# Kernel tuning notes

Measured on AMD Instinct MI355X. Metric: run time of the kernel, lower is better.

The kernel has to match this reference:

```python
import jax, jax.numpy as jnp
import numpy as np

V, OOV, E, HE, HD, N, S, TD = 50000, 50, 256, 512, 512, 32, 400, 30
PAD_INF = -1e10


def _gru_step(h, x, Wih, Whh, bih, bhh):
    gi = x @ Wih.T + bih            # [N,3H]
    gh = h @ Whh.T + bhh
    ir, iz, inn = jnp.split(gi, 3, axis=-1)
    hr, hz, hn = jnp.split(gh, 3, axis=-1)
    r = jax.nn.sigmoid(ir + hr)
    z = jax.nn.sigmoid(iz + hz)
    n = jnp.tanh(inn + r * hn)
    return (1.0 - z) * n + z * h


def setup_inputs() -> dict:
    key = jax.random.key(0)
    ks = iter(jax.random.split(key, 40))
    def rn(shape, s=0.05):
        return s * jax.random.normal(next(ks), shape, dtype=jnp.float32)
    return {
        "src_ids": jax.random.randint(next(ks), (N, S), 0, V),
        "src_mask": jnp.ones((N, S), jnp.float32),
        "trg_ids": jax.random.randint(next(ks), (N, TD), 0, V),
        "ptr_src_idx": jax.random.randint(next(ks), (N, S), 0, V + OOV),
        "embed": rn((V, E), 0.1),
        "Wih_f": rn((3 * HE, E)), "Whh_f": rn((3 * HE, HE)),
        "bih_f": rn((3 * HE,)), "bhh_f": rn((3 * HE,)),
        "Wih_b": rn((3 * HE, E)), "Whh_b": rn((3 * HE, HE)),
        "bih_b": rn((3 * HE,)), "bhh_b": rn((3 * HE,)),
        "Wih_d": rn((3 * HD, E)), "Whh_d": rn((3 * HD, HD)),
        "bih_d": rn((3 * HD,)), "bhh_d": rn((3 * HD,)),
        "Wk": rn((2 * HE, HD)), "Wd": rn((HD, HD)), "battn": rn((HD,)), "v": rn((HD,)),
        "W1": rn((2 * HE + HD, HD)), "b1": rn((HD,)),
        "W2": rn((HD, V)), "b2": rn((V,)),
        "Wp": rn((2 * HE + HD + E, 1)), "bp": rn((1,)),
    }


def reference(src_ids, src_mask, trg_ids, ptr_src_idx, embed,
              Wih_f, Whh_f, bih_f, bhh_f, Wih_b, Whh_b, bih_b, bhh_b,
              Wih_d, Whh_d, bih_d, bhh_d, Wk, Wd, battn, v,
              W1, b1, W2, b2, Wp, bp):
    n = src_ids.shape[0]
    # ---- bidirectional GRU encoder ----
    xt = jnp.swapaxes(embed[src_ids], 0, 1)        # [S,N,E]
    h0 = jnp.zeros((n, HE), jnp.float32)
    def fstep(h, xi):
        h2 = _gru_step(h, xi, Wih_f, Whh_f, bih_f, bhh_f)
        return h2, h2
    def bstep(h, xi):
        h2 = _gru_step(h, xi, Wih_b, Whh_b, bih_b, bhh_b)
        return h2, h2
    _, hf = jax.lax.scan(fstep, h0, xt)
    _, hb = jax.lax.scan(bstep, h0, xt[::-1])
    enc = jnp.swapaxes(jnp.concatenate([hf, hb[::-1]], axis=-1), 0, 1)  # [N,S,2HE]

    key_proj = enc @ Wk                             # [N,S,HD] precomputed attn keys
    mask_add = (1.0 - src_mask) * PAD_INF           # [N,S]
    rows = jnp.arange(n)[:, None]

    trg_emb = jnp.swapaxes(embed[trg_ids], 0, 1)    # [TD,N,E]
    hd0 = jnp.zeros((n, HD), jnp.float32)

    def dstep(h, xi):
        h = _gru_step(h, xi, Wih_d, Whh_d, bih_d, bhh_d)
        # additive attention
        e = jnp.tanh(key_proj + (h @ Wd + battn)[:, None, :]) @ v + mask_add  # [N,S]
        attn = jax.nn.softmax(e, axis=-1)
        ctx = jnp.einsum('ns,nsd->nd', attn, enc)                # [N,2HE]
        concat = jnp.concatenate([h, ctx], axis=-1)              # [N,2HE+HD]
        gen = jax.nn.softmax((concat @ W1 + b1) @ W2 + b2, axis=-1)  # [N,V]
        gen_ext = jnp.concatenate([gen, jnp.zeros((n, OOV), gen.dtype)], axis=-1)
        p_gen = jax.nn.sigmoid(jnp.concatenate([xi, ctx, h], axis=-1) @ Wp + bp)  # [N,1]
        out = (p_gen * gen_ext).at[rows, ptr_src_idx].add((1.0 - p_gen) * attn)
        return h, out

    _, dists = jax.lax.scan(dstep, hd0, trg_emb)    # [TD,N,V+OOV]
    return jnp.swapaxes(dists, 0, 1)                # [N,TD,V+OOV]
```

## Files before the change

kernel.cpp:

```cpp
#include <hip/hip_runtime.h>
#include <math.h>

#define VSZ 50000
#define OOVN 50
#define VE 50050
#define EMB 256
#define HE 512
#define HD 512
#define NB 32
#define SRC 400
#define TDD 30
#define G3 1536
#define ENC_PER_DIR 128
#define DEC_NBLK 128

__device__ __forceinline__ float sigmf(float x) { return 1.f / (1.f + expf(-x)); }

__global__ __launch_bounds__(256) void transpose_kernel(const float* __restrict__ in,
                                                        float* __restrict__ out,
                                                        int rows, int cols) {
    int idx = blockIdx.x * 256 + threadIdx.x;
    if (idx >= rows * cols) return;
    int r = idx / cols, c = idx % cols;
    out[c * rows + r] = in[idx];
}

__global__ __launch_bounds__(256) void gi_kernel(const int* __restrict__ ids,
                                                 const float* __restrict__ embed,
                                                 const float* __restrict__ WihT,
                                                 const float* __restrict__ bih,
                                                 float* __restrict__ gi, int steps) {
    __shared__ float sx[16][EMB];
    __shared__ int stok[16];
    int tid = threadIdx.x;
    int g0 = blockIdx.x * 16;
    if (tid < 16) {
        int row = g0 + tid;
        int s = row / NB, n = row % NB;
        stok[tid] = ids[n * steps + s];
    }
    __syncthreads();
    for (int r = 0; r < 16; ++r) sx[r][tid] = embed[(size_t)stok[r] * EMB + tid];
    __syncthreads();
    int c = blockIdx.y * 256 + tid;
    float b = bih[c];
    float acc[16];
#pragma unroll
    for (int r = 0; r < 16; ++r) acc[r] = b;
    for (int e = 0; e < EMB; e += 4) {
        float w0 = WihT[(size_t)(e + 0) * G3 + c];
        float w1 = WihT[(size_t)(e + 1) * G3 + c];
        float w2 = WihT[(size_t)(e + 2) * G3 + c];
        float w3 = WihT[(size_t)(e + 3) * G3 + c];
#pragma unroll
        for (int r = 0; r < 16; ++r) {
            float4 x4 = *(const float4*)&sx[r][e];
            acc[r] += x4.x * w0 + x4.y * w1 + x4.z * w2 + x4.w * w3;
        }
    }
#pragma unroll
    for (int r = 0; r < 16; ++r) gi[(size_t)(g0 + r) * G3 + c] = acc[r];
}

__global__ __launch_bounds__(512) void enc_scan_kernel(
    const float* __restrict__ giF, const float* __restrict__ giB,
    const float* __restrict__ WhhF, const float* __restrict__ WhhB,
    const float* __restrict__ bhhF, const float* __restrict__ bhhB,
    float* __restrict__ hF0, float* __restrict__ hF1,
    float* __restrict__ hB0, float* __restrict__ hB1,
    float* __restrict__ enc, unsigned int* __restrict__ cnt) {
    const int bid = blockIdx.x;
    const int z = bid >> 7;
    const int j0 = (bid & 127) * 4;
    const float* gi  = z ? giB : giF;
    const float* Whh = z ? WhhB : WhhF;
    const float* bhh = z ? bhhB : bhhF;
    float* hbuf[2];
    hbuf[0] = z ? hB0 : hF0;
    hbuf[1] = z ? hB1 : hF1;
    unsigned int* cntd = cnt + (size_t)z * 512;

    __shared__ float hlds[32 * 576];

    const int tid = threadIdx.x;
    const int jl = tid & 3;
    const int kh = (tid >> 2) & 15;
    const int ng = tid >> 6;
    const int j  = j0 + jl;
    const int kbase = kh * 36;

    float4 wreg[3][8];
#pragma unroll
    for (int g = 0; g < 3; ++g) {
        const float* wp = Whh + (size_t)(g * 512 + j) * 512 + kh * 32;
#pragma unroll
        for (int i = 0; i < 8; ++i) wreg[g][i] = *(const float4*)&wp[i * 4];
    }
    const float bR = bhh[j], bZ = bhh[512 + j], bN = bhh[1024 + j];

    for (int t = 0; t < SRC; ++t) {
        const float* hin = hbuf[t & 1];
        float* hout = hbuf[(t + 1) & 1];
        const unsigned long long* hin8 = (const unsigned long long*)hin;
        for (int idx = tid; idx < 32 * 256; idx += 512) {
            unsigned long long uv = __hip_atomic_load(&hin8[idx], __ATOMIC_RELAXED,
                                                      __HIP_MEMORY_SCOPE_AGENT);
            union { unsigned long long u; float f[2]; } cv; cv.u = uv;
            int nn = idx >> 8, kk = (idx & 255) << 1;
            int off = nn * 576 + (kk >> 5) * 36 + (kk & 31);
            hlds[off] = cv.f[0];
            hlds[off + 1] = cv.f[1];
        }
        __syncthreads();

        float aR[4] = {0.f, 0.f, 0.f, 0.f};
        float aZ[4] = {0.f, 0.f, 0.f, 0.f};
        float aN[4] = {0.f, 0.f, 0.f, 0.f};
        const float* h0p = &hlds[(ng * 4 + 0) * 576 + kbase];
        const float* h1p = &hlds[(ng * 4 + 1) * 576 + kbase];
        const float* h2p = &hlds[(ng * 4 + 2) * 576 + kbase];
        const float* h3p = &hlds[(ng * 4 + 3) * 576 + kbase];
#pragma unroll
        for (int i = 0; i < 8; ++i) {
            float4 wr = wreg[0][i], wz = wreg[1][i], wn = wreg[2][i];
            float4 ha = *(const float4*)&h0p[i * 4];
            float4 hb = *(const float4*)&h1p[i * 4];
            float4 hc = *(const float4*)&h2p[i * 4];
            float4 hd = *(const float4*)&h3p[i * 4];
            aR[0] += ha.x*wr.x + ha.y*wr.y + ha.z*wr.z + ha.w*wr.w;
            aZ[0] += ha.x*wz.x + ha.y*wz.y + ha.z*wz.z + ha.w*wz.w;
            aN[0] += ha.x*wn.x + ha.y*wn.y + ha.z*wn.z + ha.w*wn.w;
            aR[1] += hb.x*wr.x + hb.y*wr.y + hb.z*wr.z + hb.w*wr.w;
            aZ[1] += hb.x*wz.x + hb.y*wz.y + hb.z*wz.z + hb.w*wz.w;
            aN[1] += hb.x*wn.x + hb.y*wn.y + hb.z*wn.z + hb.w*wn.w;
            aR[2] += hc.x*wr.x + hc.y*wr.y + hc.z*wr.z + hc.w*wr.w;
            aZ[2] += hc.x*wz.x + hc.y*wz.y + hc.z*wz.z + hc.w*wz.w;
            aN[2] += hc.x*wn.x + hc.y*wn.y + hc.z*wn.z + hc.w*wn.w;
            aR[3] += hd.x*wr.x + hd.y*wr.y + hd.z*wr.z + hd.w*wr.w;
            aZ[3] += hd.x*wz.x + hd.y*wz.y + hd.z*wz.z + hd.w*wz.w;
            aN[3] += hd.x*wn.x + hd.y*wn.y + hd.z*wn.z + hd.w*wn.w;
        }
#pragma unroll
        for (int r = 0; r < 4; ++r) {
            aR[r] += __shfl_xor(aR[r], 4);  aR[r] += __shfl_xor(aR[r], 8);
            aR[r] += __shfl_xor(aR[r], 16); aR[r] += __shfl_xor(aR[r], 32);
            aZ[r] += __shfl_xor(aZ[r], 4);  aZ[r] += __shfl_xor(aZ[r], 8);
            aZ[r] += __shfl_xor(aZ[r], 16); aZ[r] += __shfl_xor(aZ[r], 32);
            aN[r] += __shfl_xor(aN[r], 4);  aN[r] += __shfl_xor(aN[r], 8);
            aN[r] += __shfl_xor(aN[r], 16); aN[r] += __shfl_xor(aN[r], 32);
        }
        if (kh == 0) {
            int s = z ? (SRC - 1 - t) : t;
#pragma unroll
            for (int r = 0; r < 4; ++r) {
                int n = ng * 4 + r;
                const float* gir = gi + (size_t)(s * NB + n) * G3;
                float rr  = sigmf(gir[j] + bR + aR[r]);
                float zz  = sigmf(gir[512 + j] + bZ + aZ[r]);
                float nn2 = tanhf(gir[1024 + j] + bN + rr * aN[r]);
                float hp  = hlds[n * 576 + (j >> 5) * 36 + (j & 31)];
                float hnew = (1.f - zz) * nn2 + zz * hp;
                __hip_atomic_store(&hout[n * 512 + j], hnew, __ATOMIC_RELAXED,
                                   __HIP_MEMORY_SCOPE_AGENT);
                enc[(size_t)(n * SRC + s) * 1024 + z * 512 + j] = hnew;
            }
        }
        __syncthreads();
        if (tid == 0) {
            __hip_atomic_fetch_add(&cntd[t], 1u, __ATOMIC_RELAXED, __HIP_MEMORY_SCOPE_AGENT);
            while (__hip_atomic_load(&cntd[t], __ATOMIC_RELAXED, __HIP_MEMORY_SCOPE_AGENT)
                   < (unsigned)ENC_PER_DIR)
                __builtin_amdgcn_s_sleep(2);
        }
        __syncthreads();
    }
}

__global__ __launch_bounds__(512) void dec_scan_kernel(
    const float* __restrict__ gi, const float* __restrict__ Whh,
    const float* __restrict__ bhh, const float* __restrict__ h0,
    float* __restrict__ hall, unsigned int* __restrict__ cnt) {
    const int j0 = blockIdx.x * 4;
    __shared__ float hlds[32 * 576];
    const int tid = threadIdx.x;
    const int jl = tid & 3;
    const int kh = (tid >> 2) & 15;
    const int ng = tid >> 6;
    const int j  = j0 + jl;
    const int kbase = kh * 36;

    float4 wreg[3][8];
#pragma unroll
    for (int g = 0; g < 3; ++g) {
        const float* wp = Whh + (size_t)(g * 512 + j) * 512 + kh * 32;
#pragma unroll
        for (int i = 0; i < 8; ++i) wreg[g][i] = *(const float4*)&wp[i * 4];
    }
    const float bR = bhh[j], bZ = bhh[512 + j], bN = bhh[1024 + j];

    for (int t = 0; t < TDD; ++t) {
        const float* hin = t ? (hall + (size_t)(t - 1) * NB * 512) : h0;
        float* hout = hall + (size_t)t * NB * 512;
        const unsigned long long* hin8 = (const unsigned long long*)hin;
        for (int idx = tid; idx < 32 * 256; idx += 512) {
            unsigned long long uv = __hip_atomic_load(&hin8[idx], __ATOMIC_RELAXED,
                                                      __HIP_MEMORY_SCOPE_AGENT);
            union { unsigned long long u; float f[2]; } cv; cv.u = uv;
            int nn = idx >> 8, kk = (idx & 255) << 1;
            int off = nn * 576 + (kk >> 5) * 36 + (kk & 31);
            hlds[off] = cv.f[0];
            hlds[off + 1] = cv.f[1];
        }
        __syncthreads();

        float aR[4] = {0.f, 0.f, 0.f, 0.f};
        float aZ[4] = {0.f, 0.f, 0.f, 0.f};
        float aN[4] = {0.f, 0.f, 0.f, 0.f};
        const float* h0p = &hlds[(ng * 4 + 0) * 576 + kbase];
        const float* h1p = &hlds[(ng * 4 + 1) * 576 + kbase];
        const float* h2p = &hlds[(ng * 4 + 2) * 576 + kbase];
        const float* h3p = &hlds[(ng * 4 + 3) * 576 + kbase];
#pragma unroll
        for (int i = 0; i < 8; ++i) {
            float4 wr = wreg[0][i], wz = wreg[1][i], wn = wreg[2][i];
            float4 ha = *(const float4*)&h0p[i * 4];
            float4 hb = *(const float4*)&h1p[i * 4];
            float4 hc = *(const float4*)&h2p[i * 4];
            float4 hd = *(const float4*)&h3p[i * 4];
            aR[0] += ha.x*wr.x + ha.y*wr.y + ha.z*wr.z + ha.w*wr.w;
            aZ[0] += ha.x*wz.x + ha.y*wz.y + ha.z*wz.z + ha.w*wz.w;
            aN[0] += ha.x*wn.x + ha.y*wn.y + ha.z*wn.z + ha.w*wn.w;
            aR[1] += hb.x*wr.x + hb.y*wr.y + hb.z*wr.z + hb.w*wr.w;
            aZ[1] += hb.x*wz.x + hb.y*wz.y + hb.z*wz.z + hb.w*wz.w;
            aN[1] += hb.x*wn.x + hb.y*wn.y + hb.z*wn.z + hb.w*wn.w;
            aR[2] += hc.x*wr.x + hc.y*wr.y + hc.z*wr.z + hc.w*wr.w;
            aZ[2] += hc.x*wz.x + hc.y*wz.y + hc.z*wz.z + hc.w*wz.w;
            aN[2] += hc.x*wn.x + hc.y*wn.y + hc.z*wn.z + hc.w*wn.w;
            aR[3] += hd.x*wr.x + hd.y*wr.y + hd.z*wr.z + hd.w*wr.w;
            aZ[3] += hd.x*wz.x + hd.y*wz.y + hd.z*wz.z + hd.w*wz.w;
            aN[3] += hd.x*wn.x + hd.y*wn.y + hd.z*wn.z + hd.w*wn.w;
        }
#pragma unroll
        for (int r = 0; r < 4; ++r) {
            aR[r] += __shfl_xor(aR[r], 4);  aR[r] += __shfl_xor(aR[r], 8);
            aR[r] += __shfl_xor(aR[r], 16); aR[r] += __shfl_xor(aR[r], 32);
            aZ[r] += __shfl_xor(aZ[r], 4);  aZ[r] += __shfl_xor(aZ[r], 8);
            aZ[r] += __shfl_xor(aZ[r], 16); aZ[r] += __shfl_xor(aZ[r], 32);
            aN[r] += __shfl_xor(aN[r], 4);  aN[r] += __shfl_xor(aN[r], 8);
            aN[r] += __shfl_xor(aN[r], 16); aN[r] += __shfl_xor(aN[r], 32);
        }
        if (kh == 0) {
#pragma unroll
            for (int r = 0; r < 4; ++r) {
                int n = ng * 4 + r;
                const float* gir = gi + (size_t)(t * NB + n) * G3;
                float rr  = sigmf(gir[j] + bR + aR[r]);
                float zz  = sigmf(gir[512 + j] + bZ + aZ[r]);
                float nn2 = tanhf(gir[1024 + j] + bN + rr * aN[r]);
                float hp  = hlds[n * 576 + (j >> 5) * 36 + (j & 31)];
                float hnew = (1.f - zz) * nn2 + zz * hp;
                __hip_atomic_store(&hout[n * 512 + j], hnew, __ATOMIC_RELAXED,
                                   __HIP_MEMORY_SCOPE_AGENT);
            }
        }
        __syncthreads();
        if (tid == 0) {
            __hip_atomic_fetch_add(&cnt[t], 1u, __ATOMIC_RELAXED, __HIP_MEMORY_SCOPE_AGENT);
            while (__hip_atomic_load(&cnt[t], __ATOMIC_RELAXED, __HIP_MEMORY_SCOPE_AGENT)
                   < (unsigned)DEC_NBLK)
                __builtin_amdgcn_s_sleep(2);
        }
        __syncthreads();
    }
}

__global__ __launch_bounds__(256) void keyproj_kernel(const float* __restrict__ enc,
                                                      const float* __restrict__ Wk,
                                                      float* __restrict__ kp) {
    __shared__ float sx[8][1024];
    int tid = threadIdx.x;
    int g0 = blockIdx.x * 8;
    for (int i = tid; i < 8 * 1024; i += 256)
        sx[i >> 10][i & 1023] = enc[(size_t)(g0 + (i >> 10)) * 1024 + (i & 1023)];
    __syncthreads();
    int c = blockIdx.y * 256 + tid;
    float acc[8];
#pragma unroll
    for (int r = 0; r < 8; ++r) acc[r] = 0.f;
    for (int k = 0; k < 1024; k += 4) {
        float w0 = Wk[(size_t)(k + 0) * 512 + c];
        float w1 = Wk[(size_t)(k + 1) * 512 + c];
        float w2 = Wk[(size_t)(k + 2) * 512 + c];
        float w3 = Wk[(size_t)(k + 3) * 512 + c];
#pragma unroll
        for (int r = 0; r < 8; ++r) {
            float4 x4 = *(const float4*)&sx[r][k];
            acc[r] += x4.x * w0 + x4.y * w1 + x4.z * w2 + x4.w * w3;
        }
    }
#pragma unroll
    for (int r = 0; r < 8; ++r) kp[(size_t)(g0 + r) * 512 + c] = acc[r];
}

__global__ __launch_bounds__(256) void qall_kernel(const float* __restrict__ hall,
                                                   const float* __restrict__ Wd,
                                                   const float* __restrict__ battn,
                                                   float* __restrict__ qall) {
    __shared__ float sx[8][512];
    int tid = threadIdx.x;
    int g0 = blockIdx.x * 8;
    for (int i = tid; i < 8 * 512; i += 256)
        sx[i >> 9][i & 511] = hall[(size_t)(g0 + (i >> 9)) * 512 + (i & 511)];
    __syncthreads();
    int c = blockIdx.y * 256 + tid;
    float b = battn[c];
    float acc[8];
#pragma unroll
    for (int r = 0; r < 8; ++r) acc[r] = b;
    for (int k = 0; k < 512; k += 4) {
        float w0 = Wd[(size_t)(k + 0) * 512 + c];
        float w1 = Wd[(size_t)(k + 1) * 512 + c];
        float w2 = Wd[(size_t)(k + 2) * 512 + c];
        float w3 = Wd[(size_t)(k + 3) * 512 + c];
#pragma unroll
        for (int r = 0; r < 8; ++r) {
            float4 x4 = *(const float4*)&sx[r][k];
            acc[r] += x4.x * w0 + x4.y * w1 + x4.z * w2 + x4.w * w3;
        }
    }
#pragma unroll
    for (int r = 0; r < 8; ++r) qall[(size_t)(g0 + r) * 512 + c] = acc[r];
}

__global__ __launch_bounds__(256) void escoreall_kernel(const float* __restrict__ kp,
                                                        const float* __restrict__ qall,
                                                        const float* __restrict__ vvec,
                                                        const float* __restrict__ mask,
                                                        float* __restrict__ e) {
    __shared__ float sq[512];
    int tid = threadIdx.x;
    int row0 = blockIdx.x * 4;
    int tn = row0 / SRC;
    int n = tn % NB;
    sq[tid] = qall[(size_t)tn * 512 + tid];
    sq[256 + tid] = qall[(size_t)tn * 512 + 256 + tid];
    __syncthreads();
    int w = tid >> 6, lane = tid & 63;
    int row = row0 + w;
    int s = row % SRC;
    const float* kpr = kp + (size_t)(n * SRC + s) * 512;
    float acc = 0.f;
#pragma unroll
    for (int i = 0; i < 8; ++i) {
        int d = lane + i * 64;
        acc += vvec[d] * tanhf(kpr[d] + sq[d]);
    }
    for (int off = 32; off; off >>= 1) acc += __shfl_down(acc, off, 64);
    if (lane == 0) e[row] = acc + (1.f - mask[n * SRC + s]) * (-1e10f);
}

__global__ __launch_bounds__(256) void softmaxS_kernel(float* __restrict__ e) {
    __shared__ float red[256];
    int n = blockIdx.x, tid = threadIdx.x;
    float* row = e + (size_t)n * SRC;
    float m = -3.4e38f;
    for (int s = tid; s < SRC; s += 256) m = fmaxf(m, row[s]);
    red[tid] = m; __syncthreads();
    for (int off = 128; off; off >>= 1) { if (tid < off) red[tid] = fmaxf(red[tid], red[tid + off]); __syncthreads(); }
    m = red[0]; __syncthreads();
    float sum = 0.f;
    for (int s = tid; s < SRC; s += 256) sum += expf(row[s] - m);
    red[tid] = sum; __syncthreads();
    for (int off = 128; off; off >>= 1) { if (tid < off) red[tid] += red[tid + off]; __syncthreads(); }
    float inv = 1.f / red[0]; __syncthreads();
    for (int s = tid; s < SRC; s += 256) row[s] = expf(row[s] - m) * inv;
}

__global__ __launch_bounds__(256) void ctxall_kernel(const float* __restrict__ attn,
                                                     const float* __restrict__ enc,
                                                     float* __restrict__ ctxall) {
    __shared__ float sa[TDD * SRC];
    int n = blockIdx.x, tid = threadIdx.x;
    for (int i = tid; i < TDD * SRC; i += 256) {
        int t = i / SRC, s = i - t * SRC;
        sa[i] = attn[(size_t)(t * NB + n) * SRC + s];
    }
    __syncthreads();
    int d = blockIdx.y * 256 + tid;
    const float* er = enc + (size_t)n * SRC * 1024 + d;
    float acc[TDD];
#pragma unroll
    for (int t = 0; t < TDD; ++t) acc[t] = 0.f;
    for (int s = 0; s < SRC; s += 4) {
        float e0 = er[(size_t)(s + 0) * 1024];
        float e1 = er[(size_t)(s + 1) * 1024];
        float e2 = er[(size_t)(s + 2) * 1024];
        float e3 = er[(size_t)(s + 3) * 1024];
#pragma unroll
        for (int t = 0; t < TDD; ++t) {
            float4 a4 = *(const float4*)&sa[t * SRC + s];
            acc[t] += a4.x * e0 + a4.y * e1 + a4.z * e2 + a4.w * e3;
        }
    }
#pragma unroll
    for (int t = 0; t < TDD; ++t) ctxall[(size_t)(t * NB + n) * 1024 + d] = acc[t];
}

__global__ __launch_bounds__(256) void pgenall_kernel(const int* __restrict__ trg_ids,
                                                      const float* __restrict__ embed,
                                                      const float* __restrict__ ctxall,
                                                      const float* __restrict__ hall,
                                                      const float* __restrict__ Wp,
                                                      const float* __restrict__ bp,
                                                      float* __restrict__ pgenall) {
    __shared__ float red[256];
    int tn = blockIdx.x, tid = threadIdx.x;
    int t = tn / NB, n = tn % NB;
    int tok = trg_ids[n * TDD + t];
    float acc = 0.f;
    for (int i = tid; i < 1792; i += 256) {
        float val;
        if (i < 256) val = embed[(size_t)tok * EMB + i];
        else if (i < 1280) val = ctxall[(size_t)tn * 1024 + (i - 256)];
        else val = hall[(size_t)tn * 512 + (i - 1280)];
        acc += val * Wp[i];
    }
    red[tid] = acc; __syncthreads();
    for (int off = 128; off; off >>= 1) { if (tid < off) red[tid] += red[tid + off]; __syncthreads(); }
    if (tid == 0) pgenall[tn] = 1.f / (1.f + expf(-(red[0] + bp[0])));
}

__global__ __launch_bounds__(256) void hid1all_kernel(const float* __restrict__ hall,
                                                      const float* __restrict__ ctxall,
                                                      const float* __restrict__ W1,
                                                      const float* __restrict__ b1,
                                                      float* __restrict__ hid1all) {
    __shared__ float sc[8][1536];
    int tid = threadIdx.x;
    int g0 = blockIdx.x * 8;
    for (int i = tid; i < 8 * 512; i += 256)
        sc[i >> 9][i & 511] = hall[(size_t)(g0 + (i >> 9)) * 512 + (i & 511)];
    for (int i = tid; i < 8 * 1024; i += 256)
        sc[i >> 10][512 + (i & 1023)] = ctxall[(size_t)(g0 + (i >> 10)) * 1024 + (i & 1023)];
    __syncthreads();
    int c = blockIdx.y * 256 + tid;
    float acc[8];
    float b = b1[c];
#pragma unroll
    for (int r = 0; r < 8; ++r) acc[r] = b;
    for (int k = 0; k < 1536; k += 4) {
        float w0 = W1[(size_t)(k + 0) * 512 + c];
        float w1 = W1[(size_t)(k + 1) * 512 + c];
        float w2 = W1[(size_t)(k + 2) * 512 + c];
        float w3 = W1[(size_t)(k + 3) * 512 + c];
#pragma unroll
        for (int r = 0; r < 8; ++r) {
            float4 x4 = *(const float4*)&sc[r][k];
            acc[r] += x4.x * w0 + x4.y * w1 + x4.z * w2 + x4.w * w3;
        }
    }
#pragma unroll
    for (int r = 0; r < 8; ++r) hid1all[(size_t)(g0 + r) * 512 + c] = acc[r];
}

__global__ __launch_bounds__(256) void logitsall_kernel(const float* __restrict__ hid1,
                                                        const float* __restrict__ W2,
                                                        const float* __restrict__ b2,
                                                        float* __restrict__ logits) {
    __shared__ float sh[32][512];
    int tid = threadIdx.x;
    int r0 = blockIdx.y * 32;
    for (int i = tid; i < 32 * 512; i += 256) sh[i >> 9][i & 511] = hid1[(size_t)r0 * 512 + i];
    __syncthreads();
    int j = blockIdx.x * 256 + tid;
    if (j >= VSZ) return;
    float acc[32];
#pragma unroll
    for (int r = 0; r < 32; ++r) acc[r] = 0.f;
    for (int k = 0; k < 512; k += 4) {
        float w0 = W2[(size_t)(k + 0) * VSZ + j];
        float w1 = W2[(size_t)(k + 1) * VSZ + j];
        float w2 = W2[(size_t)(k + 2) * VSZ + j];
        float w3 = W2[(size_t)(k + 3) * VSZ + j];
#pragma unroll
        for (int r = 0; r < 32; ++r) {
            float4 h4 = *(const float4*)&sh[r][k];
            acc[r] += h4.x * w0 + h4.y * w1 + h4.z * w2 + h4.w * w3;
        }
    }
    float bb = b2[j];
#pragma unroll
    for (int r = 0; r < 32; ++r) logits[(size_t)(r0 + r) * VSZ + j] = acc[r] + bb;
}

__global__ __launch_bounds__(1024) void outall_kernel(const float* __restrict__ logits,
                                                      const float* __restrict__ pgenall,
                                                      float* __restrict__ out) {
    __shared__ float red[1024];
    int tn = blockIdx.x, tid = threadIdx.x;
    int t = tn / NB, n = tn % NB;
    const float* lrow = logits + (size_t)tn * VSZ;
    float m = -3.4e38f;
    for (int j = tid; j < VSZ; j += 1024) m = fmaxf(m, lrow[j]);
    red[tid] = m; __syncthreads();
    for (int off = 512; off; off >>= 1) { if (tid < off) red[tid] = fmaxf(red[tid], red[tid + off]); __syncthreads(); }
    m = red[0]; __syncthreads();
    float sum = 0.f;
    for (int j = tid; j < VSZ; j += 1024) sum += expf(lrow[j] - m);
    red[tid] = sum; __syncthreads();
    for (int off = 512; off; off >>= 1) { if (tid < off) red[tid] += red[tid + off]; __syncthreads(); }
    float inv = pgenall[tn] / red[0];
    float* orow = out + (size_t)(n * TDD + t) * VE;
    for (int j = tid; j < VE; j += 1024) orow[j] = (j < VSZ) ? expf(lrow[j] - m) * inv : 0.f;
}

__global__ __launch_bounds__(256) void scatterall_kernel(const int* __restrict__ ptr,
                                                         const float* __restrict__ attn,
                                                         const float* __restrict__ pgenall,
                                                         float* __restrict__ out) {
    int f = blockIdx.x * 256 + threadIdx.x;
    if (f >= TDD * NB * SRC) return;
    int tn = f / SRC;
    int s = f - tn * SRC;
    int t = tn / NB, n = tn % NB;
    float w = (1.f - pgenall[tn]) * attn[f];
    atomicAdd(&out[(size_t)(n * TDD + t) * VE + ptr[n * SRC + s]], w);
}

extern "C" void kernel_launch(void* const* d_in, const int* in_sizes, int n_in,
                              void* d_out, int out_size, void* d_ws, size_t ws_size,
                              hipStream_t stream) {
    const int*   src_ids  = (const int*)d_in[0];
    const float* src_mask = (const float*)d_in[1];
    const int*   trg_ids  = (const int*)d_in[2];
    const int*   ptr_idx  = (const int*)d_in[3];
    const float* embed    = (const float*)d_in[4];
    const float* Wih_f = (const float*)d_in[5];
    const float* Whh_f = (const float*)d_in[6];
    const float* bih_f = (const float*)d_in[7];
    const float* bhh_f = (const float*)d_in[8];
    const float* Wih_b = (const float*)d_in[9];
    const float* Whh_b = (const float*)d_in[10];
    const float* bih_b = (const float*)d_in[11];
    const float* bhh_b = (const float*)d_in[12];
    const float* Wih_d = (const float*)d_in[13];
    const float* Whh_d = (const float*)d_in[14];
    const float* bih_d = (const float*)d_in[15];
    const float* bhh_d = (const float*)d_in[16];
    const float* Wk    = (const float*)d_in[17];
    const float* Wd    = (const float*)d_in[18];
    const float* battn = (const float*)d_in[19];
    const float* vvec  = (const float*)d_in[20];
    const float* W1    = (const float*)d_in[21];
    const float* b1    = (const float*)d_in[22];
    const float* W2    = (const float*)d_in[23];
    const float* b2    = (const float*)d_in[24];
    const float* Wp    = (const float*)d_in[25];
    const float* bp    = (const float*)d_in[26];
    float* out = (float*)d_out;

    float* w = (float*)d_ws;
    float* WihTf = w; w += 256 * G3;
    float* WihTb = w; w += 256 * G3;
    float* WihTd = w; w += 256 * G3;
    float* giF = w; w += (size_t)SRC * NB * G3;
    float* giB = w; w += (size_t)SRC * NB * G3;
    float* giD = w; w += (size_t)TDD * NB * G3;
    float* enc = w; w += (size_t)NB * SRC * 1024;
    float* kp  = w; w += (size_t)NB * SRC * 512;
    float* hF0 = w; w += NB * HE;
    float* hF1 = w; w += NB * HE;
    float* hB0 = w; w += NB * HE;
    float* hB1 = w; w += NB * HE;
    float* h0d = w; w += NB * HD;
    float* hD_all = w; w += (size_t)TDD * NB * HD;
    float* q_all  = w; w += (size_t)TDD * NB * 512;
    float* e_all  = w; w += (size_t)TDD * NB * SRC;
    float* ctx_all = w; w += (size_t)TDD * NB * 1024;
    float* hid1_all = w; w += (size_t)TDD * NB * 512;
    float* pgen_all = w; w += 1024;
    unsigned int* cnt = (unsigned int*)w; w += 2048;
    float* logits_all = giF;

    transpose_kernel<<<(G3 * 256 + 255) / 256, 256, 0, stream>>>(Wih_f, WihTf, G3, 256);
    transpose_kernel<<<(G3 * 256 + 255) / 256, 256, 0, stream>>>(Wih_b, WihTb, G3, 256);
    transpose_kernel<<<(G3 * 256 + 255) / 256, 256, 0, stream>>>(Wih_d, WihTd, G3, 256);

    gi_kernel<<<dim3(SRC * NB / 16, 6), 256, 0, stream>>>(src_ids, embed, WihTf, bih_f, giF, SRC);
    gi_kernel<<<dim3(SRC * NB / 16, 6), 256, 0, stream>>>(src_ids, embed, WihTb, bih_b, giB, SRC);
    gi_kernel<<<dim3(TDD * NB / 16, 6), 256, 0, stream>>>(trg_ids, embed, WihTd, bih_d, giD, TDD);

    hipMemsetAsync(hF0, 0, NB * HE * sizeof(float), stream);
    hipMemsetAsync(hB0, 0, NB * HE * sizeof(float), stream);
    hipMemsetAsync(h0d, 0, NB * HD * sizeof(float), stream);
    hipMemsetAsync(cnt, 0, 2048 * sizeof(unsigned int), stream);

    enc_scan_kernel<<<2 * ENC_PER_DIR, 512, 0, stream>>>(
        giF, giB, Whh_f, Whh_b, bhh_f, bhh_b,
        hF0, hF1, hB0, hB1, enc, cnt);

    keyproj_kernel<<<dim3(NB * SRC / 8, 2), 256, 0, stream>>>(enc, Wk, kp);

    dec_scan_kernel<<<DEC_NBLK, 512, 0, stream>>>(giD, Whh_d, bhh_d, h0d, hD_all, cnt + 1024);

    qall_kernel<<<dim3(TDD * NB / 8, 2), 256, 0, stream>>>(hD_all, Wd, battn, q_all);
    escoreall_kernel<<<TDD * NB * SRC / 4, 256, 0, stream>>>(kp, q_all, vvec, src_mask, e_all);
    softmaxS_kernel<<<TDD * NB, 256, 0, stream>>>(e_all);
    ctxall_kernel<<<dim3(NB, 4), 256, 0, stream>>>(e_all, enc, ctx_all);
    pgenall_kernel<<<TDD * NB, 256, 0, stream>>>(trg_ids, embed, ctx_all, hD_all, Wp, bp, pgen_all);
    hid1all_kernel<<<dim3(TDD * NB / 8, 2), 256, 0, stream>>>(hD_all, ctx_all, W1, b1, hid1_all);
    logitsall_kernel<<<dim3((VSZ + 255) / 256, TDD), 256, 0, stream>>>(hid1_all, W2, b2, logits_all);
    outall_kernel<<<TDD * NB, 1024, 0, stream>>>(logits_all, pgen_all, out);
    scatterall_kernel<<<(TDD * NB * SRC + 255) / 256, 256, 0, stream>>>(ptr_idx, e_all, pgen_all, out);
}
```

Baseline: 8.734 ms.

## Fuse encoder and decoder GRU scans into one persistent kernel; vectorize projections

```diff
diff --git a/kernel.cpp b/kernel.cpp
--- a/kernel.cpp
+++ b/kernel.cpp
@@ -11,8 +11,7 @@
 #define SRC 400
 #define TDD 30
 #define G3 1536
-#define ENC_PER_DIR 128
-#define DEC_NBLK 128
+#define FSCAN_NBLK 128
 
 __device__ __forceinline__ float sigmf(float x) { return 1.f / (1.f + expf(-x)); }
 
@@ -62,215 +61,174 @@
     for (int r = 0; r < 16; ++r) gi[(size_t)(g0 + r) * G3 + c] = acc[r];
 }
 
-__global__ __launch_bounds__(512) void enc_scan_kernel(
+template <int MODE>
+__device__ __forceinline__ void gru_phase(
+    const float* __restrict__ hin,
+    const float* __restrict__ gibase,
+    const float* __restrict__ Whh,
+    float bR, float bZ, float bN,
+    float* __restrict__ hout,
+    float* __restrict__ aux,
+    int s,
+    float* __restrict__ hlds,
+    int tid, int jl, int kh, int ng, int j) {
+    float gpre[12];
+    if (kh == 0) {
+#pragma unroll
+        for (int r = 0; r < 4; ++r) {
+            const float* gir = gibase + (size_t)(ng * 4 + r) * G3 + j;
+            gpre[r * 3 + 0] = gir[0];
+            gpre[r * 3 + 1] = gir[512];
+            gpre[r * 3 + 2] = gir[1024];
+        }
+    }
+    float4 wreg[3][8];
+#pragma unroll
+    for (int g = 0; g < 3; ++g) {
+        const float* wp = Whh + (size_t)(g * 512 + j) * 512 + kh * 32;
+#pragma unroll
+        for (int i = 0; i < 8; ++i) wreg[g][i] = *(const float4*)&wp[i * 4];
+    }
+    const unsigned long long* hin8 = (const unsigned long long*)hin;
+    for (int idx = tid; idx < 32 * 256; idx += 512) {
+        unsigned long long uv = __hip_atomic_load(&hin8[idx], __ATOMIC_RELAXED,
+                                                  __HIP_MEMORY_SCOPE_AGENT);
+        union { unsigned long long u; float f[2]; } cv; cv.u = uv;
+        int nn = idx >> 8, kk = (idx & 255) << 1;
+        int off = nn * 576 + (kk >> 5) * 36 + (kk & 31);
+        hlds[off] = cv.f[0];
+        hlds[off + 1] = cv.f[1];
+    }
+    __syncthreads();
+
+    float aR[4] = {0.f, 0.f, 0.f, 0.f};
+    float aZ[4] = {0.f, 0.f, 0.f, 0.f};
+    float aN[4] = {0.f, 0.f, 0.f, 0.f};
+    const int kbase = kh * 36;
+    const float* h0p = &hlds[(ng * 4 + 0) * 576 + kbase];
+    const float* h1p = &hlds[(ng * 4 + 1) * 576 + kbase];
+    const float* h2p = &hlds[(ng * 4 + 2) * 576 + kbase];
+    const float* h3p = &hlds[(ng * 4 + 3) * 576 + kbase];
+#pragma unroll
+    for (int i = 0; i < 8; ++i) {
+        float4 wr = wreg[0][i], wz = wreg[1][i], wn = wreg[2][i];
+        float4 ha = *(const float4*)&h0p[i * 4];
+        float4 hb = *(const float4*)&h1p[i * 4];
+        float4 hc = *(const float4*)&h2p[i * 4];
+        float4 hd = *(const float4*)&h3p[i * 4];
+        aR[0] += ha.x*wr.x + ha.y*wr.y + ha.z*wr.z + ha.w*wr.w;
+        aZ[0] += ha.x*wz.x + ha.y*wz.y + ha.z*wz.z + ha.w*wz.w;
+        aN[0] += ha.x*wn.x + ha.y*wn.y + ha.z*wn.z + ha.w*wn.w;
+        aR[1] += hb.x*wr.x + hb.y*wr.y + hb.z*wr.z + hb.w*wr.w;
+        aZ[1] += hb.x*wz.x + hb.y*wz.y + hb.z*wz.z + hb.w*wz.w;
+        aN[1] += hb.x*wn.x + hb.y*wn.y + hb.z*wn.z + hb.w*wn.w;
+        aR[2] += hc.x*wr.x + hc.y*wr.y + hc.z*wr.z + hc.w*wr.w;
+        aZ[2] += hc.x*wz.x + hc.y*wz.y + hc.z*wz.z + hc.w*wz.w;
+        aN[2] += hc.x*wn.x + hc.y*wn.y + hc.z*wn.z + hc.w*wn.w;
+        aR[3] += hd.x*wr.x + hd.y*wr.y + hd.z*wr.z + hd.w*wr.w;
+        aZ[3] += hd.x*wz.x + hd.y*wz.y + hd.z*wz.z + hd.w*wz.w;
+        aN[3] += hd.x*wn.x + hd.y*wn.y + hd.z*wn.z + hd.w*wn.w;
+    }
+#pragma unroll
+    for (int r = 0; r < 4; ++r) {
+        aR[r] += __shfl_xor(aR[r], 4);  aR[r] += __shfl_xor(aR[r], 8);
+        aR[r] += __shfl_xor(aR[r], 16); aR[r] += __shfl_xor(aR[r], 32);
+        aZ[r] += __shfl_xor(aZ[r], 4);  aZ[r] += __shfl_xor(aZ[r], 8);
+        aZ[r] += __shfl_xor(aZ[r], 16); aZ[r] += __shfl_xor(aZ[r], 32);
+        aN[r] += __shfl_xor(aN[r], 4);  aN[r] += __shfl_xor(aN[r], 8);
+        aN[r] += __shfl_xor(aN[r], 16); aN[r] += __shfl_xor(aN[r], 32);
+    }
+    if (kh == 0) {
+#pragma unroll
+        for (int r = 0; r < 4; ++r) {
+            int n = ng * 4 + r;
+            float rr  = sigmf(gpre[r * 3 + 0] + bR + aR[r]);
+            float zz  = sigmf(gpre[r * 3 + 1] + bZ + aZ[r]);
+            float nn2 = tanhf(gpre[r * 3 + 2] + bN + rr * aN[r]);
+            float hp  = hlds[n * 576 + (j >> 5) * 36 + (j & 31)];
+            float hnew = (1.f - zz) * nn2 + zz * hp;
+            __hip_atomic_store(&hout[n * 512 + j], hnew, __ATOMIC_RELAXED,
+                               __HIP_MEMORY_SCOPE_AGENT);
+            if (MODE == 0)      aux[(size_t)(n * SRC + s) * 1024 + j] = hnew;
+            else if (MODE == 1) aux[(size_t)(n * SRC + s) * 1024 + 512 + j] = hnew;
+            else                aux[n * 512 + j] = hnew;
+        }
+    }
+    __syncthreads();
+}
+
+__global__ __launch_bounds__(512) void fused_scan_kernel(
     const float* __restrict__ giF, const float* __restrict__ giB,
+    const float* __restrict__ giD,
     const float* __restrict__ WhhF, const float* __restrict__ WhhB,
+    const float* __restrict__ WhhD,
     const float* __restrict__ bhhF, const float* __restrict__ bhhB,
+    const float* __restrict__ bhhD,
     float* __restrict__ hF0, float* __restrict__ hF1,
     float* __restrict__ hB0, float* __restrict__ hB1,
-    float* __restrict__ enc, unsigned int* __restrict__ cnt) {
+    float* __restrict__ h0d, float* __restrict__ hDs,
+    float* __restrict__ hD_all, float* __restrict__ enc,
+    unsigned int* __restrict__ flags) {
     const int bid = blockIdx.x;
-    const int z = bid >> 7;
-    const int j0 = (bid & 127) * 4;
-    const float* gi  = z ? giB : giF;
-    const float* Whh = z ? WhhB : WhhF;
-    const float* bhh = z ? bhhB : bhhF;
-    float* hbuf[2];
-    hbuf[0] = z ? hB0 : hF0;
-    hbuf[1] = z ? hB1 : hF1;
-    unsigned int* cntd = cnt + (size_t)z * 512;
-
-    __shared__ float hlds[32 * 576];
-
-    const int tid = threadIdx.x;
-    const int jl = tid & 3;
-    const int kh = (tid >> 2) & 15;
-    const int ng = tid >> 6;
-    const int j  = j0 + jl;
-    const int kbase = kh * 36;
-
-    float4 wreg[3][8];
-#pragma unroll
-    for (int g = 0; g < 3; ++g) {
-        const float* wp = Whh + (size_t)(g * 512 + j) * 512 + kh * 32;
-#pragma unroll
-        for (int i = 0; i < 8; ++i) wreg[g][i] = *(const float4*)&wp[i * 4];
-    }
-    const float bR = bhh[j], bZ = bhh[512 + j], bN = bhh[1024 + j];
-
-    for (int t = 0; t < SRC; ++t) {
-        const float* hin = hbuf[t & 1];
-        float* hout = hbuf[(t + 1) & 1];
-        const unsigned long long* hin8 = (const unsigned long long*)hin;
-        for (int idx = tid; idx < 32 * 256; idx += 512) {
-            unsigned long long uv = __hip_atomic_load(&hin8[idx], __ATOMIC_RELAXED,
-                                                      __HIP_MEMORY_SCOPE_AGENT);
-            union { unsigned long long u; float f[2]; } cv; cv.u = uv;
-            int nn = idx >> 8, kk = (idx & 255) << 1;
-            int off = nn * 576 + (kk >> 5) * 36 + (kk & 31);
-            hlds[off] = cv.f[0];
-            hlds[off + 1] = cv.f[1];
-        }
-        __syncthreads();
-
-        float aR[4] = {0.f, 0.f, 0.f, 0.f};
-        float aZ[4] = {0.f, 0.f, 0.f, 0.f};
-        float aN[4] = {0.f, 0.f, 0.f, 0.f};
-        const float* h0p = &hlds[(ng * 4 + 0) * 576 + kbase];
-        const float* h1p = &hlds[(ng * 4 + 1) * 576 + kbase];
-        const float* h2p = &hlds[(ng * 4 + 2) * 576 + kbase];
-        const float* h3p = &hlds[(ng * 4 + 3) * 576 + kbase];
-#pragma unroll
-        for (int i = 0; i < 8; ++i) {
-            float4 wr = wreg[0][i], wz = wreg[1][i], wn = wreg[2][i];
-            float4 ha = *(const float4*)&h0p[i * 4];
-            float4 hb = *(const float4*)&h1p[i * 4];
-            float4 hc = *(const float4*)&h2p[i * 4];
-            float4 hd = *(const float4*)&h3p[i * 4];
-            aR[0] += ha.x*wr.x + ha.y*wr.y + ha.z*wr.z + ha.w*wr.w;
-            aZ[0] += ha.x*wz.x + ha.y*wz.y + ha.z*wz.z + ha.w*wz.w;
-            aN[0] += ha.x*wn.x + ha.y*wn.y + ha.z*wn.z + ha.w*wn.w;
-            aR[1] += hb.x*wr.x + hb.y*wr.y + hb.z*wr.z + hb.w*wr.w;
-            aZ[1] += hb.x*wz.x + hb.y*wz.y + hb.z*wz.z + hb.w*wz.w;
-            aN[1] += hb.x*wn.x + hb.y*wn.y + hb.z*wn.z + hb.w*wn.w;
-            aR[2] += hc.x*wr.x + hc.y*wr.y + hc.z*wr.z + hc.w*wr.w;
-            aZ[2] += hc.x*wz.x + hc.y*wz.y + hc.z*wz.z + hc.w*wz.w;
-            aN[2] += hc.x*wn.x + hc.y*wn.y + hc.z*wn.z + hc.w*wn.w;
-            aR[3] += hd.x*wr.x + hd.y*wr.y + hd.z*wr.z + hd.w*wr.w;
-            aZ[3] += hd.x*wz.x + hd.y*wz.y + hd.z*wz.z + hd.w*wz.w;
-            aN[3] += hd.x*wn.x + hd.y*wn.y + hd.z*wn.z + hd.w*wn.w;
-        }
-#pragma unroll
-        for (int r = 0; r < 4; ++r) {
-            aR[r] += __shfl_xor(aR[r], 4);  aR[r] += __shfl_xor(aR[r], 8);
-            aR[r] += __shfl_xor(aR[r], 16); aR[r] += __shfl_xor(aR[r], 32);
-            aZ[r] += __shfl_xor(aZ[r], 4);  aZ[r] += __shfl_xor(aZ[r], 8);
-            aZ[r] += __shfl_xor(aZ[r], 16); aZ[r] += __shfl_xor(aZ[r], 32);
-            aN[r] += __shfl_xor(aN[r], 4);  aN[r] += __shfl_xor(aN[r], 8);
-            aN[r] += __shfl_xor(aN[r], 16); aN[r] += __shfl_xor(aN[r], 32);
-        }
-        if (kh == 0) {
-            int s = z ? (SRC - 1 - t) : t;
-#pragma unroll
-            for (int r = 0; r < 4; ++r) {
-                int n = ng * 4 + r;
-                const float* gir = gi + (size_t)(s * NB + n) * G3;
-                float rr  = sigmf(gir[j] + bR + aR[r]);
-                float zz  = sigmf(gir[512 + j] + bZ + aZ[r]);
-                float nn2 = tanhf(gir[1024 + j] + bN + rr * aN[r]);
-                float hp  = hlds[n * 576 + (j >> 5) * 36 + (j & 31)];
-                float hnew = (1.f - zz) * nn2 + zz * hp;
-                __hip_atomic_store(&hout[n * 512 + j], hnew, __ATOMIC_RELAXED,
-                                   __HIP_MEMORY_SCOPE_AGENT);
-                enc[(size_t)(n * SRC + s) * 1024 + z * 512 + j] = hnew;
-            }
-        }
-        __syncthreads();
-        if (tid == 0) {
-            __hip_atomic_fetch_add(&cntd[t], 1u, __ATOMIC_RELAXED, __HIP_MEMORY_SCOPE_AGENT);
-            while (__hip_atomic_load(&cntd[t], __ATOMIC_RELAXED, __HIP_MEMORY_SCOPE_AGENT)
-                   < (unsigned)ENC_PER_DIR)
-                __builtin_amdgcn_s_sleep(2);
-        }
-        __syncthreads();
-    }
-}
-
-__global__ __launch_bounds__(512) void dec_scan_kernel(
-    const float* __restrict__ gi, const float* __restrict__ Whh,
-    const float* __restrict__ bhh, const float* __restrict__ h0,
-    float* __restrict__ hall, unsigned int* __restrict__ cnt) {
-    const int j0 = blockIdx.x * 4;
+    const int j0 = bid * 4;
     __shared__ float hlds[32 * 576];
     const int tid = threadIdx.x;
     const int jl = tid & 3;
     const int kh = (tid >> 2) & 15;
     const int ng = tid >> 6;
     const int j  = j0 + jl;
-    const int kbase = kh * 36;
-
-    float4 wreg[3][8];
-#pragma unroll
-    for (int g = 0; g < 3; ++g) {
-        const float* wp = Whh + (size_t)(g * 512 + j) * 512 + kh * 32;
-#pragma unroll
-        for (int i = 0; i < 8; ++i) wreg[g][i] = *(const float4*)&wp[i * 4];
-    }
-    const float bR = bhh[j], bZ = bhh[512 + j], bN = bhh[1024 + j];
-
-    for (int t = 0; t < TDD; ++t) {
-        const float* hin = t ? (hall + (size_t)(t - 1) * NB * 512) : h0;
-        float* hout = hall + (size_t)t * NB * 512;
-        const unsigned long long* hin8 = (const unsigned long long*)hin;
-        for (int idx = tid; idx < 32 * 256; idx += 512) {
-            unsigned long long uv = __hip_atomic_load(&hin8[idx], __ATOMIC_RELAXED,
-                                                      __HIP_MEMORY_SCOPE_AGENT);
-            union { unsigned long long u; float f[2]; } cv; cv.u = uv;
-            int nn = idx >> 8, kk = (idx & 255) << 1;
-            int off = nn * 576 + (kk >> 5) * 36 + (kk & 31);
-            hlds[off] = cv.f[0];
-            hlds[off + 1] = cv.f[1];
-        }
-        __syncthreads();
-
-        float aR[4] = {0.f, 0.f, 0.f, 0.f};
-        float aZ[4] = {0.f, 0.f, 0.f, 0.f};
-        float aN[4] = {0.f, 0.f, 0.f, 0.f};
-        const float* h0p = &hlds[(ng * 4 + 0) * 576 + kbase];
-        const float* h1p = &hlds[(ng * 4 + 1) * 576 + kbase];
-        const float* h2p = &hlds[(ng * 4 + 2) * 576 + kbase];
-        const float* h3p = &hlds[(ng * 4 + 3) * 576 + kbase];
-#pragma unroll
-        for (int i = 0; i < 8; ++i) {
-            float4 wr = wreg[0][i], wz = wreg[1][i], wn = wreg[2][i];
-            float4 ha = *(const float4*)&h0p[i * 4];
-            float4 hb = *(const float4*)&h1p[i * 4];
-            float4 hc = *(const float4*)&h2p[i * 4];
-            float4 hd = *(const float4*)&h3p[i * 4];
-            aR[0] += ha.x*wr.x + ha.y*wr.y + ha.z*wr.z + ha.w*wr.w;
-            aZ[0] += ha.x*wz.x + ha.y*wz.y + ha.z*wz.z + ha.w*wz.w;
-            aN[0] += ha.x*wn.x + ha.y*wn.y + ha.z*wn.z + ha.w*wn.w;
-            aR[1] += hb.x*wr.x + hb.y*wr.y + hb.z*wr.z + hb.w*wr.w;
-            aZ[1] += hb.x*wz.x + hb.y*wz.y + hb.z*wz.z + hb.w*wz.w;
-            aN[1] += hb.x*wn.x + hb.y*wn.y + hb.z*wn.z + hb.w*wn.w;
-            aR[2] += hc.x*wr.x + hc.y*wr.y + hc.z*wr.z + hc.w*wr.w;
-            aZ[2] += hc.x*wz.x + hc.y*wz.y + hc.z*wz.z + hc.w*wz.w;
-            aN[2] += hc.x*wn.x + hc.y*wn.y + hc.z*wn.z + hc.w*wn.w;
-            aR[3] += hd.x*wr.x + hd.y*wr.y + hd.z*wr.z + hd.w*wr.w;
-            aZ[3] += hd.x*wz.x + hd.y*wz.y + hd.z*wz.z + hd.w*wz.w;
-            aN[3] += hd.x*wn.x + hd.y*wn.y + hd.z*wn.z + hd.w*wn.w;
-        }
-#pragma unroll
-        for (int r = 0; r < 4; ++r) {
-            aR[r] += __shfl_xor(aR[r], 4);  aR[r] += __shfl_xor(aR[r], 8);
-            aR[r] += __shfl_xor(aR[r], 16); aR[r] += __shfl_xor(aR[r], 32);
-            aZ[r] += __shfl_xor(aZ[r], 4);  aZ[r] += __shfl_xor(aZ[r], 8);
-            aZ[r] += __shfl_xor(aZ[r], 16); aZ[r] += __shfl_xor(aZ[r], 32);
-            aN[r] += __shfl_xor(aN[r], 4);  aN[r] += __shfl_xor(aN[r], 8);
-            aN[r] += __shfl_xor(aN[r], 16); aN[r] += __shfl_xor(aN[r], 32);
-        }
-        if (kh == 0) {
-#pragma unroll
-            for (int r = 0; r < 4; ++r) {
-                int n = ng * 4 + r;
-                const float* gir = gi + (size_t)(t * NB + n) * G3;
-                float rr  = sigmf(gir[j] + bR + aR[r]);
-                float zz  = sigmf(gir[512 + j] + bZ + aZ[r]);
-                float nn2 = tanhf(gir[1024 + j] + bN + rr * aN[r]);
-                float hp  = hlds[n * 576 + (j >> 5) * 36 + (j & 31)];
-                float hnew = (1.f - zz) * nn2 + zz * hp;
-                __hip_atomic_store(&hout[n * 512 + j], hnew, __ATOMIC_RELAXED,
-                                   __HIP_MEMORY_SCOPE_AGENT);
+
+    const float bFR = bhhF[j], bFZ = bhhF[512 + j], bFN = bhhF[1024 + j];
+    const float bBR = bhhB[j], bBZ = bhhB[512 + j], bBN = bhhB[1024 + j];
+    const float bDR = bhhD[j], bDZ = bhhD[512 + j], bDN = bhhD[1024 + j];
+
+    for (int t = 0; t < SRC; ++t) {
+        gru_phase<0>((t & 1) ? hF1 : hF0, giF + (size_t)t * NB * G3, WhhF,
+                     bFR, bFZ, bFN, (t & 1) ? hF0 : hF1, enc, t,
+                     hlds, tid, jl, kh, ng, j);
+        if (tid == 0)
+            __hip_atomic_store(&flags[(size_t)t * 128 + bid], 1u,
+                               __ATOMIC_RELAXED, __HIP_MEMORY_SCOPE_AGENT);
+        {
+            int sb = SRC - 1 - t;
+            gru_phase<1>((t & 1) ? hB1 : hB0, giB + (size_t)sb * NB * G3, WhhB,
+                         bBR, bBZ, bBN, (t & 1) ? hB0 : hB1, enc, sb,
+                         hlds, tid, jl, kh, ng, j);
+            if (tid == 0)
+                __hip_atomic_store(&flags[(size_t)(SRC + t) * 128 + bid], 1u,
+                                   __ATOMIC_RELAXED, __HIP_MEMORY_SCOPE_AGENT);
+        }
+        if (t < TDD) {
+            gru_phase<2>(t ? (hDs + (size_t)(t - 1) * NB * 512) : h0d,
+                         giD + (size_t)t * NB * G3, WhhD,
+                         bDR, bDZ, bDN, hDs + (size_t)t * NB * 512,
+                         hD_all + (size_t)t * NB * 512, 0,
+                         hlds, tid, jl, kh, ng, j);
+            if (tid == 0)
+                __hip_atomic_store(&flags[(size_t)(2 * SRC + t) * 128 + bid], 1u,
+                                   __ATOMIC_RELAXED, __HIP_MEMORY_SCOPE_AGENT);
+        }
+        if (t != SRC - 1) {
+            if (tid < 64) {
+                const unsigned int* fF = flags + (size_t)t * 128;
+                const unsigned int* fB = flags + (size_t)(SRC + t) * 128;
+                const unsigned int* fD = flags + (size_t)(2 * SRC + t) * 128;
+                const int pd = (t < TDD);
+                for (;;) {
+                    unsigned int a = __hip_atomic_load(&fF[tid], __ATOMIC_RELAXED, __HIP_MEMORY_SCOPE_AGENT)
+                                   & __hip_atomic_load(&fF[64 + tid], __ATOMIC_RELAXED, __HIP_MEMORY_SCOPE_AGENT)
+                                   & __hip_atomic_load(&fB[tid], __ATOMIC_RELAXED, __HIP_MEMORY_SCOPE_AGENT)
+                                   & __hip_atomic_load(&fB[64 + tid], __ATOMIC_RELAXED, __HIP_MEMORY_SCOPE_AGENT);
+                    if (pd) {
+                        a &= __hip_atomic_load(&fD[tid], __ATOMIC_RELAXED, __HIP_MEMORY_SCOPE_AGENT)
+                           & __hip_atomic_load(&fD[64 + tid], __ATOMIC_RELAXED, __HIP_MEMORY_SCOPE_AGENT);
+                    }
+                    if (__all(a != 0u)) break;
+                    __builtin_amdgcn_s_sleep(1);
+                }
             }
-        }
-        __syncthreads();
-        if (tid == 0) {
-            __hip_atomic_fetch_add(&cnt[t], 1u, __ATOMIC_RELAXED, __HIP_MEMORY_SCOPE_AGENT);
-            while (__hip_atomic_load(&cnt[t], __ATOMIC_RELAXED, __HIP_MEMORY_SCOPE_AGENT)
-                   < (unsigned)DEC_NBLK)
-                __builtin_amdgcn_s_sleep(2);
-        }
-        __syncthreads();
+            __syncthreads();
+        }
     }
 }
 
@@ -283,23 +241,25 @@
     for (int i = tid; i < 8 * 1024; i += 256)
         sx[i >> 10][i & 1023] = enc[(size_t)(g0 + (i >> 10)) * 1024 + (i & 1023)];
     __syncthreads();
-    int c = blockIdx.y * 256 + tid;
-    float acc[8];
-#pragma unroll
-    for (int r = 0; r < 8; ++r) acc[r] = 0.f;
+    int c = tid * 2;
+    float acc[8][2];
+#pragma unroll
+    for (int r = 0; r < 8; ++r) { acc[r][0] = 0.f; acc[r][1] = 0.f; }
     for (int k = 0; k < 1024; k += 4) {
-        float w0 = Wk[(size_t)(k + 0) * 512 + c];
-        float w1 = Wk[(size_t)(k + 1) * 512 + c];
-        float w2 = Wk[(size_t)(k + 2) * 512 + c];
-        float w3 = Wk[(size_t)(k + 3) * 512 + c];
+        float2 w0 = *(const float2*)&Wk[(size_t)(k + 0) * 512 + c];
+        float2 w1 = *(const float2*)&Wk[(size_t)(k + 1) * 512 + c];
+        float2 w2 = *(const float2*)&Wk[(size_t)(k + 2) * 512 + c];
+        float2 w3 = *(const float2*)&Wk[(size_t)(k + 3) * 512 + c];
 #pragma unroll
         for (int r = 0; r < 8; ++r) {
             float4 x4 = *(const float4*)&sx[r][k];
-            acc[r] += x4.x * w0 + x4.y * w1 + x4.z * w2 + x4.w * w3;
-        }
-    }
-#pragma unroll
-    for (int r = 0; r < 8; ++r) kp[(size_t)(g0 + r) * 512 + c] = acc[r];
+            acc[r][0] += x4.x * w0.x + x4.y * w1.x + x4.z * w2.x + x4.w * w3.x;
+            acc[r][1] += x4.x * w0.y + x4.y * w1.y + x4.z * w2.y + x4.w * w3.y;
+        }
+    }
+#pragma unroll
+    for (int r = 0; r < 8; ++r)
+        *(float2*)&kp[(size_t)(g0 + r) * 512 + c] = make_float2(acc[r][0], acc[r][1]);
 }
 
 __global__ __launch_bounds__(256) void qall_kernel(const float* __restrict__ hall,
@@ -467,30 +427,38 @@
                                                         const float* __restrict__ W2,
                                                         const float* __restrict__ b2,
                                                         float* __restrict__ logits) {
-    __shared__ float sh[32][512];
+    __shared__ float sh[16][512];
     int tid = threadIdx.x;
-    int r0 = blockIdx.y * 32;
-    for (int i = tid; i < 32 * 512; i += 256) sh[i >> 9][i & 511] = hid1[(size_t)r0 * 512 + i];
-    __syncthreads();
-    int j = blockIdx.x * 256 + tid;
+    int r0 = blockIdx.y * 16;
+    for (int i = tid; i < 16 * 512; i += 256) sh[i >> 9][i & 511] = hid1[(size_t)r0 * 512 + i];
+    __syncthreads();
+    int j = blockIdx.x * 1024 + tid * 4;
     if (j >= VSZ) return;
-    float acc[32];
-#pragma unroll
-    for (int r = 0; r < 32; ++r) acc[r] = 0.f;
+    float acc[16][4];
+#pragma unroll
+    for (int r = 0; r < 16; ++r) { acc[r][0]=0.f; acc[r][1]=0.f; acc[r][2]=0.f; acc[r][3]=0.f; }
     for (int k = 0; k < 512; k += 4) {
-        float w0 = W2[(size_t)(k + 0) * VSZ + j];
-        float w1 = W2[(size_t)(k + 1) * VSZ + j];
-        float w2 = W2[(size_t)(k + 2) * VSZ + j];
-        float w3 = W2[(size_t)(k + 3) * VSZ + j];
-#pragma unroll
-        for (int r = 0; r < 32; ++r) {
+        float4 w0 = *(const float4*)&W2[(size_t)(k + 0) * VSZ + j];
+        float4 w1 = *(const float4*)&W2[(size_t)(k + 1) * VSZ + j];
+        float4 w2 = *(const float4*)&W2[(size_t)(k + 2) * VSZ + j];
+        float4 w3 = *(const float4*)&W2[(size_t)(k + 3) * VSZ + j];
+#pragma unroll
+        for (int r = 0; r < 16; ++r) {
             float4 h4 = *(const float4*)&sh[r][k];
-            acc[r] += h4.x * w0 + h4.y * w1 + h4.z * w2 + h4.w * w3;
-        }
-    }
-    float bb = b2[j];
-#pragma unroll
-    for (int r = 0; r < 32; ++r) logits[(size_t)(r0 + r) * VSZ + j] = acc[r] + bb;
+            acc[r][0] += h4.x * w0.x + h4.y * w1.x + h4.z * w2.x + h4.w * w3.x;
+            acc[r][1] += h4.x * w0.y + h4.y * w1.y + h4.z * w2.y + h4.w * w3.y;
+            acc[r][2] += h4.x * w0.z + h4.y * w1.z + h4.z * w2.z + h4.w * w3.z;
+            acc[r][3] += h4.x * w0.w + h4.y * w1.w + h4.z * w2.w + h4.w * w3.w;
+        }
+    }
+    float4 bb = *(const float4*)&b2[j];
+#pragma unroll
+    for (int r = 0; r < 16; ++r) {
+        float4 o;
+        o.x = acc[r][0] + bb.x; o.y = acc[r][1] + bb.y;
+        o.z = acc[r][2] + bb.z; o.w = acc[r][3] + bb.w;
+        *(float4*)&logits[(size_t)(r0 + r) * VSZ + j] = o;
+    }
 }
 
 __global__ __launch_bounds__(1024) void outall_kernel(const float* __restrict__ logits,
@@ -501,17 +469,17 @@
     int t = tn / NB, n = tn % NB;
     const float* lrow = logits + (size_t)tn * VSZ;
     float m = -3.4e38f;
-    for (int j = tid; j < VSZ; j += 1024) m = fmaxf(m, lrow[j]);
+    for (int jj = tid; jj < VSZ; jj += 1024) m = fmaxf(m, lrow[jj]);
     red[tid] = m; __syncthreads();
     for (int off = 512; off; off >>= 1) { if (tid < off) red[tid] = fmaxf(red[tid], red[tid + off]); __syncthreads(); }
     m = red[0]; __syncthreads();
     float sum = 0.f;
-    for (int j = tid; j < VSZ; j += 1024) sum += expf(lrow[j] - m);
+    for (int jj = tid; jj < VSZ; jj += 1024) sum += expf(lrow[jj] - m);
     red[tid] = sum; __syncthreads();
     for (int off = 512; off; off >>= 1) { if (tid < off) red[tid] += red[tid + off]; __syncthreads(); }
     float inv = pgenall[tn] / red[0];
     float* orow = out + (size_t)(n * TDD + t) * VE;
-    for (int j = tid; j < VE; j += 1024) orow[j] = (j < VSZ) ? expf(lrow[j] - m) * inv : 0.f;
+    for (int jj = tid; jj < VE; jj += 1024) orow[jj] = (jj < VSZ) ? expf(lrow[jj] - m) * inv : 0.f;
 }
 
 __global__ __launch_bounds__(256) void scatterall_kernel(const int* __restrict__ ptr,
@@ -565,7 +533,7 @@
     float* WihTd = w; w += 256 * G3;
     float* giF = w; w += (size_t)SRC * NB * G3;
     float* giB = w; w += (size_t)SRC * NB * G3;
-    float* giD = w; w += (size_t)TDD * NB * G3;
+    float* giD = w; w += (size_t)SRC * NB * G3;
     float* enc = w; w += (size_t)NB * SRC * 1024;
     float* kp  = w; w += (size_t)NB * SRC * 512;
     float* hF0 = w; w += NB * HE;
@@ -573,13 +541,14 @@
     float* hB0 = w; w += NB * HE;
     float* hB1 = w; w += NB * HE;
     float* h0d = w; w += NB * HD;
+    float* hDs = w; w += (size_t)TDD * NB * HD;
     float* hD_all = w; w += (size_t)TDD * NB * HD;
     float* q_all  = w; w += (size_t)TDD * NB * 512;
     float* e_all  = w; w += (size_t)TDD * NB * SRC;
     float* ctx_all = w; w += (size_t)TDD * NB * 1024;
     float* hid1_all = w; w += (size_t)TDD * NB * 512;
     float* pgen_all = w; w += 1024;
-    unsigned int* cnt = (unsigned int*)w; w += 2048;
+    unsigned int* flags = (unsigned int*)w; w += (2 * SRC + TDD) * 128;
     float* logits_all = giF;
 
     transpose_kernel<<<(G3 * 256 + 255) / 256, 256, 0, stream>>>(Wih_f, WihTf, G3, 256);
@@ -593,15 +562,13 @@
     hipMemsetAsync(hF0, 0, NB * HE * sizeof(float), stream);
     hipMemsetAsync(hB0, 0, NB * HE * sizeof(float), stream);
     hipMemsetAsync(h0d, 0, NB * HD * sizeof(float), stream);
-    hipMemsetAsync(cnt, 0, 2048 * sizeof(unsigned int), stream);
-
-    enc_scan_kernel<<<2 * ENC_PER_DIR, 512, 0, stream>>>(
-        giF, giB, Whh_f, Whh_b, bhh_f, bhh_b,
-        hF0, hF1, hB0, hB1, enc, cnt);
-
-    keyproj_kernel<<<dim3(NB * SRC / 8, 2), 256, 0, stream>>>(enc, Wk, kp);
-
-    dec_scan_kernel<<<DEC_NBLK, 512, 0, stream>>>(giD, Whh_d, bhh_d, h0d, hD_all, cnt + 1024);
+    hipMemsetAsync(flags, 0, (2 * SRC + TDD) * 128 * sizeof(unsigned int), stream);
+
+    fused_scan_kernel<<<FSCAN_NBLK, 512, 0, stream>>>(
+        giF, giB, giD, Whh_f, Whh_b, Whh_d, bhh_f, bhh_b, bhh_d,
+        hF0, hF1, hB0, hB1, h0d, hDs, hD_all, enc, flags);
+
+    keyproj_kernel<<<NB * SRC / 8, 256, 0, stream>>>(enc, Wk, kp);
 
     qall_kernel<<<dim3(TDD * NB / 8, 2), 256, 0, stream>>>(hD_all, Wd, battn, q_all);
     escoreall_kernel<<<TDD * NB * SRC / 4, 256, 0, stream>>>(kp, q_all, vvec, src_mask, e_all);
@@ -609,7 +576,7 @@
     ctxall_kernel<<<dim3(NB, 4), 256, 0, stream>>>(e_all, enc, ctx_all);
     pgenall_kernel<<<TDD * NB, 256, 0, stream>>>(trg_ids, embed, ctx_all, hD_all, Wp, bp, pgen_all);
     hid1all_kernel<<<dim3(TDD * NB / 8, 2), 256, 0, stream>>>(hD_all, ctx_all, W1, b1, hid1_all);
-    logitsall_kernel<<<dim3((VSZ + 255) / 256, TDD), 256, 0, stream>>>(hid1_all, W2, b2, logits_all);
+    logitsall_kernel<<<dim3((VSZ + 1023) / 1024, TDD * NB / 16), 256, 0, stream>>>(hid1_all, W2, b2, logits_all);
     outall_kernel<<<TDD * NB, 1024, 0, stream>>>(logits_all, pgen_all, out);
     scatterall_kernel<<<(TDD * NB * SRC + 255) / 256, 256, 0, stream>>>(ptr_idx, e_all, pgen_all, out);
 }
```

Result: slower. 16.47 ms (+88.6%).
